# Performance work log

Measured on AMD Instinct MI355X. Metric: run time of the kernel, lower is better.

Reference implementation:

```python
import jax, jax.numpy as jnp
import numpy as np

N, E, G = 2048, 65536, 32
F_ATOM, LAT, IN, ED, NB, L = 16, 64, 128, 32, 5, 5


def setup_inputs() -> dict:
    key = jax.random.key(0)
    ks = iter(jax.random.split(key, 64))
    nxt = lambda: next(ks)
    def w(shape):
        fan_in = shape[-2] if len(shape) >= 2 else 1
        return jax.random.normal(nxt(), shape, jnp.float32) / np.sqrt(fan_in)
    inp = {}
    inp['x'] = jax.random.normal(nxt(), (N, F_ATOM), jnp.float32)
    inp['t'] = jax.random.uniform(nxt(), (G, 1), jnp.float32)
    inp['z'] = jax.random.normal(nxt(), (N, LAT), jnp.float32)
    inp['edge_index'] = jax.random.randint(nxt(), (2, E), 0, N, jnp.int32)
    inp['edge_attr'] = jax.random.normal(nxt(), (E, NB), jnp.float32)
    inp['batch'] = jnp.sort(jax.random.randint(nxt(), (N,), 0, G, jnp.int32))
    inp['batch_edge_global'] = jax.random.randint(nxt(), (E,), 0, G, jnp.int32)
    # top-level dense layers
    inp['Wt_a'] = w((1, IN)); inp['bt_a'] = jnp.zeros((IN,))
    inp['Wt_b'] = w((1, ED)); inp['bt_b'] = jnp.zeros((ED,))
    inp['W_atom'] = w((F_ATOM, IN)); inp['b_atom'] = jnp.zeros((IN,))
    inp['W_bond'] = w((NB, ED)); inp['b_bond'] = jnp.zeros((ED,))
    inp['W_lat'] = w((LAT, IN)); inp['b_lat'] = jnp.zeros((IN,))
    inp['W_at'] = w((IN, IN)); inp['b_at'] = jnp.zeros((IN,))
    inp['W_bt'] = w((ED, ED)); inp['b_bt'] = jnp.zeros((ED,))
    # TopoEdgeGNN: L layers of edge-conditioned message passing with edge update
    inp['Wmsg'] = w((L, 2 * IN + ED, IN)); inp['bmsg'] = jnp.zeros((L, IN))
    inp['Wnode'] = w((L, 2 * IN, IN)); inp['bnode'] = jnp.zeros((L, IN))
    inp['Wedge'] = w((L, 2 * IN + ED, ED)); inp['bedge'] = jnp.zeros((L, ED))
    # prediction head
    inp['Wsh'] = w((IN, IN)); inp['bsh'] = jnp.zeros((IN,))
    inp['Wbm'] = w((ED, IN)); inp['bbm'] = jnp.zeros((IN,))
    inp['Wbl'] = w((IN, NB)); inp['bbl'] = jnp.zeros((NB,))
    inp['Wal'] = w((IN, F_ATOM + LAT)); inp['bal'] = jnp.zeros((F_ATOM + LAT,))
    return inp


def reference(x, t, z, edge_index, edge_attr, batch, batch_edge_global,
              Wt_a, bt_a, Wt_b, bt_b, W_atom, b_atom, W_bond, b_bond,
              W_lat, b_lat, W_at, b_at, W_bt, b_bt,
              Wmsg, bmsg, Wnode, bnode, Wedge, bedge,
              Wsh, bsh, Wbm, bbm, Wbl, bbl, Wal, bal):
    j, i = edge_index[0], edge_index[1]
    # time embeddings, gathered to nodes / edges
    ta = t @ Wt_a + bt_a            # [G, IN]
    tb = t @ Wt_b + bt_b            # [G, ED]
    tnode = ta[batch]               # [N, IN]
    tedge = tb[batch_edge_global]   # [E, ED]
    # node features
    s = x @ W_atom + b_atom
    s = (s + tnode) @ W_at + b_at
    s = s + (z @ W_lat + b_lat)
    # edge features
    e = edge_attr @ W_bond + b_bond
    e = (e + tedge) @ W_bt + b_bt
    # TopoEdgeGNN: message passing with residual node/edge updates
    for l in range(L):
        m = jax.nn.silu(jnp.concatenate([s[i], s[j], e], -1) @ Wmsg[l] + bmsg[l])  # [E, IN]
        agg = jax.ops.segment_sum(m, i, num_segments=N)                            # [N, IN]
        s = s + jax.nn.silu(jnp.concatenate([s, agg], -1) @ Wnode[l] + bnode[l])
        e = e + jax.nn.silu(jnp.concatenate([s[i], s[j], e], -1) @ Wedge[l] + bedge[l])
    # prediction head
    s2 = jax.nn.silu(s @ Wsh + bsh)
    al = s2 @ Wal + bal
    atoms_pred, latent_pred = al[:, :F_ATOM], al[:, F_ATOM:]
    # dense edge symmetrization: scatter edges into [N, N, ED], symmetrize, gather back
    e_dense = jnp.zeros((N, N, ED), e.dtype).at[j, i].set(e)
    e_dense = 0.5 * (e_dense + e_dense.transpose(1, 0, 2))
    e_sym = e_dense[j, i]           # [E, ED]
    f = jax.nn.silu(s2[i] + s2[j] + (e_sym @ Wbm + bbm))
    bonds_pred = f @ Wbl + bbl
    return latent_pred, atoms_pred, bonds_pred
```

## Files before the change

kernel.cpp:

```cpp
#include <hip/hip_runtime.h>
#include <hip/hip_bf16.h>

#define NN 2048
#define NE 65536
#define NG 32
#define CIN 128
#define CED 32
#define CLAT 64
#define CFA 16
#define CNB 5
#define NL 5

#define OFF_AT (NN * CLAT)
#define OFF_B  (NN * CLAT + NN * CFA)

typedef __attribute__((ext_vector_type(8))) short bf16x8;
typedef __attribute__((ext_vector_type(4))) float f32x4;

__device__ __forceinline__ float silu_f(float v) { return v / (1.0f + __expf(-v)); }
__device__ __forceinline__ short f2bs(float v) {
    __hip_bfloat16 h = __float2bfloat16(v);
    return *reinterpret_cast<short*>(&h);
}
__device__ __forceinline__ float bs2f(short s) {
    return __bfloat162float(*reinterpret_cast<__hip_bfloat16*>(&s));
}
__device__ __forceinline__ unsigned pack2(float a, float b) {
    return ((unsigned)(unsigned short)f2bs(b) << 16) | (unsigned short)f2bs(a);
}
__device__ __forceinline__ unsigned addpack(unsigned ua, unsigned va) {
    float a0 = bs2f((short)(ua & 0xffff)), a1 = bs2f((short)(ua >> 16));
    float b0 = bs2f((short)(va & 0xffff)), b1 = bs2f((short)(va >> 16));
    return pack2(a0 + b0, a1 + b1);
}

struct KArgs {
    const float *x, *t, *z;
    const int *jj, *ii;
    const float *ea;
    const int *batch, *beg;
    const float *Wt_a, *bt_a, *Wt_b, *bt_b, *W_atom, *b_atom, *W_bond, *b_bond;
    const float *W_lat, *b_lat, *W_at, *b_at, *W_bt, *b_bt;
    const float *Wmsg, *bmsg, *Wnode, *bnode, *Wedge, *bedge;
    const float *Wsh, *bsh, *Wbm, *bbm, *Wbl, *bbl, *Wal, *bal;
    float *s, *e;
    float *agg;
    int *cnt, *pflag, *eflag, *rowpos, *rowstart, *invp, *i_s, *j_s;
    short *s2, *U, *V, *P, *Q;
    int *map;
    short *Wpn, *Wpsh, *Wpal, *Wpbm, *Wproj, *W3m, *We3;
    float *out;
};

__device__ __forceinline__ void phase_pack(const KArgs& a, int start, int stride)
{
    for (int idx = start; idx < 6 * 4 * 20 * 64 * 8; idx += stride) {
        int j = idx & 7, t0 = idx >> 3, lane = t0 & 63, tt = t0 >> 6;
        int kq = (lane >> 4) * 8 + j, n16 = lane & 15;
        if (idx < NL * 8 * 8 * 64 * 8) {
            int nt = tt & 7, kt = (tt >> 3) & 7, l = tt >> 6;
            a.Wpn[idx] = f2bs(a.Wnode[((size_t)l * 256 + kt * 32 + kq) * CIN + nt * 16 + n16]);
        }
        if (idx < 4 * 8 * 64 * 8) {
            int nt = tt & 7, kt = tt >> 3;
            a.Wpsh[idx] = f2bs(a.Wsh[(size_t)(kt * 32 + kq) * CIN + nt * 16 + n16]);
        }
        if (idx < 4 * 5 * 64 * 8) {
            int nt = tt % 5, kt = tt / 5;
            a.Wpal[idx] = f2bs(a.Wal[(size_t)(kt * 32 + kq) * 80 + nt * 16 + n16]);
        }
        if (idx < 8 * 64 * 8) {
            int nt = tt & 7;
            a.Wpbm[idx] = f2bs(a.Wbm[(size_t)kq * CIN + nt * 16 + n16]);
        }
        {
            int nt = tt % 20; int t2 = tt / 20; int kt = t2 & 3; int slot = t2 >> 2;
            int k = kt * 32 + kq;
            float v;
            if (nt < 16) {
                int msgl = slot % 5;
                int srcK = (nt < 8) ? k : 128 + k;
                int col = (nt & 7) * 16 + n16;
                v = a.Wmsg[((size_t)msgl * 288 + srcK) * CIN + col];
            } else {
                int edgel = (slot == 0) ? 0 : slot - 1;
                int srcK = (nt < 18) ? k : 128 + k;
                int col = (nt & 1) * 16 + n16;
                v = a.Wedge[((size_t)edgel * 288 + srcK) * CED + col];
            }
            a.Wproj[idx] = f2bs(v);
        }
        if (idx < NL * 8 * 64 * 8) {
            int nt = tt & 7, l = tt >> 3;
            a.W3m[idx] = f2bs(a.Wmsg[((size_t)l * 288 + 256 + kq) * CIN + nt * 16 + n16]);
        }
        if (idx < NL * 2 * 64 * 8) {
            int nt = tt & 1, l = tt >> 1;
            a.We3[idx] = f2bs(a.Wedge[((size_t)l * 288 + 256 + kq) * CED + nt * 16 + n16]);
        }
    }
}

__device__ __forceinline__ void phase_init_s(const KArgs& a, char* smem, int tile, int tid)
{
    float* xs  = (float*)smem;
    float* zs  = (float*)(smem + 1024);
    float* tmp = (float*)(smem + 5120);
    float* tv  = (float*)(smem + 13312);
    int nb0 = tile * 16;
    int c = tid & 127, h = tid >> 7;
    if (tid < 16 * CFA / 4) ((float4*)xs)[tid] = ((const float4*)a.x)[nb0 * (CFA / 4) + tid];
    if (tid < 16 * CLAT / 4) ((float4*)zs)[tid] = ((const float4*)a.z)[nb0 * (CLAT / 4) + tid];
    if (tid < 16) tv[tid] = a.t[a.batch[nb0 + tid]];
    __syncthreads();
    float wta = a.Wt_a[c], base0 = a.b_atom[c] + a.bt_a[c];
    float acc[8];
#pragma unroll
    for (int q = 0; q < 8; q++) acc[q] = base0 + tv[h * 8 + q] * wta;
    for (int k = 0; k < CFA; k++) {
        float w = a.W_atom[k * CIN + c];
#pragma unroll
        for (int q = 0; q < 8; q++) acc[q] += xs[(h * 8 + q) * CFA + k] * w;
    }
#pragma unroll
    for (int q = 0; q < 8; q++) tmp[(h * 8 + q) * CIN + c] = acc[q];
    __syncthreads();
    float base1 = a.b_at[c] + a.b_lat[c];
    float acc2[8];
#pragma unroll
    for (int q = 0; q < 8; q++) acc2[q] = base1;
    for (int k4 = 0; k4 < CIN / 4; k4++) {
        float w0 = a.W_at[(4 * k4 + 0) * CIN + c], w1 = a.W_at[(4 * k4 + 1) * CIN + c];
        float w2 = a.W_at[(4 * k4 + 2) * CIN + c], w3 = a.W_at[(4 * k4 + 3) * CIN + c];
#pragma unroll
        for (int q = 0; q < 8; q++) {
            float4 f = *(const float4*)&tmp[(h * 8 + q) * CIN + 4 * k4];
            acc2[q] += f.x * w0 + f.y * w1 + f.z * w2 + f.w * w3;
        }
    }
    for (int k4 = 0; k4 < CLAT / 4; k4++) {
        float w0 = a.W_lat[(4 * k4 + 0) * CIN + c], w1 = a.W_lat[(4 * k4 + 1) * CIN + c];
        float w2 = a.W_lat[(4 * k4 + 2) * CIN + c], w3 = a.W_lat[(4 * k4 + 3) * CIN + c];
#pragma unroll
        for (int q = 0; q < 8; q++) {
            float4 f = *(const float4*)&zs[(h * 8 + q) * CLAT + 4 * k4];
            acc2[q] += f.x * w0 + f.y * w1 + f.z * w2 + f.w * w3;
        }
    }
#pragma unroll
    for (int q = 0; q < 8; q++) {
        int nd = nb0 + h * 8 + q;
        a.s[(size_t)nd * CIN + c] = acc2[q];
    }
}

__device__ __forceinline__ void phase_init_e(const KArgs& a, char* smem, int tb, int tid)
{
    float* eas   = (float*)smem;
    float* tv    = (float*)(smem + 1280);
    int*   sp    = (int*)(smem + 1536);
    float* tmp   = (float*)(smem + 1792);
    float* wbt   = (float*)(smem + 10240);
    float* wbond = (float*)(smem + 14336);
    float* cb    = (float*)(smem + 14976);
    float* wtb   = (float*)(smem + 15104);
    float* bbt2  = (float*)(smem + 15232);
    int k0 = tb * 64;
    for (int idx = tid; idx < 320; idx += 256) eas[idx] = a.ea[(size_t)k0 * 5 + idx];
    if (tid < 64) { tv[tid] = a.t[a.beg[k0 + tid]]; sp[tid] = a.invp[k0 + tid]; }
    for (int idx = tid; idx < 1024; idx += 256) wbt[idx] = a.W_bt[idx];
    if (tid < 160) wbond[tid] = a.W_bond[tid];
    if (tid < 32) { cb[tid] = a.b_bond[tid] + a.bt_b[tid]; wtb[tid] = a.Wt_b[tid]; bbt2[tid] = a.b_bt[tid]; }
    __syncthreads();
    int ch = tid & 31, eg = tid >> 5;
#pragma unroll
    for (int q = 0; q < 8; q++) {
        int le = eg * 8 + q;
        float acc = cb[ch] + tv[le] * wtb[ch];
#pragma unroll
        for (int bb = 0; bb < CNB; bb++) acc += eas[le * 5 + bb] * wbond[bb * 32 + ch];
        tmp[le * 33 + ch] = acc;
    }
    __syncthreads();
#pragma unroll
    for (int q = 0; q < 8; q++) {
        int le = eg * 8 + q;
        float acc2 = bbt2[ch];
        for (int d = 0; d < 32; d++) acc2 += tmp[le * 33 + d] * wbt[d * 32 + ch];
        size_t ix = (size_t)sp[le] * CED + ch;
        a.e[ix] = acc2;
        if (ch == 0) {
            int k = k0 + le;
            atomicMax(&a.map[(size_t)a.jj[k] * NN + a.ii[k]], k);
        }
    }
}

__device__ __forceinline__ void phase_node2(
    const KArgs& a, char* smem, int tile, int tid, bool DO_NODE, bool DO_POST,
    bool LOAD_S, bool STORE_S,
    const short* Wpn_l, const float* bnode_l, const short* Wproj_slot, float (*s_reg)[4],
    const int* eflag, int gen)
{
    short* feat  = (short*)smem;
    short* feat2 = (short*)(smem + 8448);
    int nb0 = tile * 16;
    int lane = tid & 63, w = tid >> 6;
    int quad = lane >> 4, n16 = lane & 15;

    if (DO_NODE) {
        if (eflag) {
            if (tid == 0) {
                int r0 = a.rowstart[nb0];
                int ed = (nb0 + 16 < NN) ? a.rowstart[nb0 + 16] : NE;
                if (ed > r0) {
                    int t1 = (ed - 1) >> 6;
                    for (int t = r0 >> 6; t <= t1; t++)
                        while (__hip_atomic_load(&eflag[t], __ATOMIC_RELAXED, __HIP_MEMORY_SCOPE_AGENT) < gen)
                            __builtin_amdgcn_s_sleep(2);
                }
            }
            __syncthreads();
            __threadfence();
        }
#pragma unroll
        for (int n2 = 0; n2 < 2; n2++) {
            int col = (w * 2 + n2) * 16 + n16;
#pragma unroll
            for (int r = 0; r < 4; r++) {
                int row = quad * 4 + r;
                if (LOAD_S) s_reg[n2][r] = a.s[(size_t)(nb0 + row) * CIN + col];
                feat[row * 264 + col] = f2bs(s_reg[n2][r]);
            }
        }
#pragma unroll
        for (int k2 = 0; k2 < 2; k2++) {
            int idx = tid + k2 * 256;
            int kl = idx >> 5, c = idx & 31;
            size_t base = (size_t)(nb0 + kl) * 128 + c;
            float4 p0 = ((const float4*)a.agg)[base];
            float4 p1 = ((const float4*)a.agg)[base + 32];
            float4 p2 = ((const float4*)a.agg)[base + 64];
            float4 p3 = ((const float4*)a.agg)[base + 96];
            float4 v; v.x = p0.x + p1.x + p2.x + p3.x; v.y = p0.y + p1.y + p2.y + p3.y;
            v.z = p0.z + p1.z + p2.z + p3.z; v.w = p0.w + p1.w + p2.w + p3.w;
            uint2 p; p.x = pack2(v.x, v.y); p.y = pack2(v.z, v.w);
            *(uint2*)&feat[kl * 264 + 128 + 4 * c] = p;
        }
        __syncthreads();
        f32x4 acc[2];
        acc[0] = (f32x4){0.f, 0.f, 0.f, 0.f};
        acc[1] = (f32x4){0.f, 0.f, 0.f, 0.f};
        const short* fbase = feat + n16 * 264 + quad * 8;
#pragma unroll
        for (int kt = 0; kt < 8; kt++) {
            bf16x8 av = *(const bf16x8*)(fbase + kt * 32);
#pragma unroll
            for (int n2 = 0; n2 < 2; n2++) {
                int nt = w * 2 + n2;
                bf16x8 b = *(const bf16x8*)(Wpn_l + ((size_t)(kt * 8 + nt) * 64 + lane) * 8);
                acc[n2] = __builtin_amdgcn_mfma_f32_16x16x32_bf16(av, b, acc[n2], 0, 0, 0);
            }
        }
#pragma unroll
        for (int n2 = 0; n2 < 2; n2++) {
            int col = (w * 2 + n2) * 16 + n16;
            float bb = bnode_l[col];
#pragma unroll
            for (int r = 0; r < 4; r++) {
                int row = quad * 4 + r;
                float v = s_reg[n2][r] + silu_f(acc[n2][r] + bb);
                s_reg[n2][r] = v;
                if (STORE_S) a.s[(size_t)(nb0 + row) * CIN + col] = v;
                feat2[row * 136 + col] = f2bs(v);
            }
        }
        __syncthreads();
    } else {
        int kl = tid >> 4, c = tid & 15;
        const float4* sp4 = (const float4*)&a.s[(size_t)(nb0 + kl) * CIN + c * 8];
        float4 v0 = sp4[0], v1 = sp4[1];
        uint4 p; p.x = pack2(v0.x, v0.y); p.y = pack2(v0.z, v0.w);
        p.z = pack2(v1.x, v1.y); p.w = pack2(v1.z, v1.w);
        *(uint4*)&feat2[kl * 136 + c * 8] = p;
        __syncthreads();
    }

    {
        f32x4 accp[5];
#pragma unroll
        for (int t2 = 0; t2 < 5; t2++) accp[t2] = (f32x4){0.f, 0.f, 0.f, 0.f};
        const short* abase = feat2 + n16 * 136 + quad * 8;
#pragma unroll
        for (int kt = 0; kt < 4; kt++) {
            bf16x8 av = *(const bf16x8*)(abase + kt * 32);
#pragma unroll
            for (int n5 = 0; n5 < 5; n5++) {
                int nt = w * 5 + n5;
                bf16x8 b = *(const bf16x8*)(Wproj_slot + ((size_t)(kt * 20 + nt) * 64 + lane) * 8);
                accp[n5] = __builtin_amdgcn_mfma_f32_16x16x32_bf16(av, b, accp[n5], 0, 0, 0);
            }
        }
#pragma unroll
        for (int n5 = 0; n5 < 5; n5++) {
            int nt = w * 5 + n5;
#pragma unroll
            for (int r = 0; r < 4; r++) {
                int node = tile * 16 + quad * 4 + r;
                short bv = f2bs(accp[n5][r]);
                if (nt < 8)       a.U[(size_t)node * CIN + nt * 16 + n16] = bv;
                else if (nt < 16) a.V[(size_t)node * CIN + (nt - 8) * 16 + n16] = bv;
                else if (nt < 18) a.P[(size_t)node * CED + (nt - 16) * 16 + n16] = bv;
                else              a.Q[(size_t)node * CED + (nt - 18) * 16 + n16] = bv;
            }
        }
    }

    if (DO_POST) {
        short* feat_s2 = feat;
        const short* fbase = feat2 + n16 * 136 + quad * 8;
        f32x4 acc[2];
        acc[0] = (f32x4){0.f, 0.f, 0.f, 0.f};
        acc[1] = (f32x4){0.f, 0.f, 0.f, 0.f};
#pragma unroll
        for (int kt = 0; kt < 4; kt++) {
            bf16x8 av = *(const bf16x8*)(fbase + kt * 32);
#pragma unroll
            for (int n2 = 0; n2 < 2; n2++) {
                int nt = w * 2 + n2;
                bf16x8 b = *(const bf16x8*)(a.Wpsh + ((size_t)(kt * 8 + nt) * 64 + lane) * 8);
                acc[n2] = __builtin_amdgcn_mfma_f32_16x16x32_bf16(av, b, acc[n2], 0, 0, 0);
            }
        }
#pragma unroll
        for (int n2 = 0; n2 < 2; n2++) {
            int col = (w * 2 + n2) * 16 + n16;
            float bb = a.bsh[col];
#pragma unroll
            for (int r = 0; r < 4; r++) {
                int row = quad * 4 + r;
                float v = silu_f(acc[n2][r] + bb);
                short bv = f2bs(v);
                a.s2[(size_t)(nb0 + row) * CIN + col] = bv;
                feat_s2[row * 136 + col] = bv;
            }
        }
        __syncthreads();
        const short* abase2 = feat_s2 + n16 * 136 + quad * 8;
        f32x4 acca[2];
        acca[0] = (f32x4){0.f, 0.f, 0.f, 0.f};
        acca[1] = (f32x4){0.f, 0.f, 0.f, 0.f};
        int nAl = (w == 0) ? 2 : 1;
        int ntl[2] = {w, 4};
#pragma unroll
        for (int kt = 0; kt < 4; kt++) {
            bf16x8 av = *(const bf16x8*)(abase2 + kt * 32);
#pragma unroll
            for (int q = 0; q < 2; q++) {
                if (q < nAl) {
                    bf16x8 b = *(const bf16x8*)(a.Wpal + ((size_t)(kt * 5 + ntl[q]) * 64 + lane) * 8);
                    acca[q] = __builtin_amdgcn_mfma_f32_16x16x32_bf16(av, b, acca[q], 0, 0, 0);
                }
            }
        }
#pragma unroll
        for (int q = 0; q < 2; q++) {
            if (q < nAl) {
                int col = ntl[q] * 16 + n16;
                float bb = a.bal[col];
#pragma unroll
                for (int r = 0; r < 4; r++) {
                    int node = nb0 + quad * 4 + r;
                    float v = acca[q][r] + bb;
                    if (col < CFA) a.out[OFF_AT + node * CFA + col] = v;
                    else           a.out[(size_t)node * CLAT + (col - CFA)] = v;
                }
            }
        }
    }
}

__device__ __forceinline__ void phase_em2(
    const KArgs& a, char* smem, int tb, int tid, bool DO_EDGE, bool DO_MSG, bool LOAD_E, bool WRITE_E,
    const short* We3p, const float* bedge_l, const short* W3mp, const float* bmsg_l,
    float (*e_reg)[4], int* eflag, int gen)
{
    short* feat_e = (short*)smem;
    short* uv_bf  = (short*)(smem + 5120);
    short* pq_bf  = (short*)(smem + 22528);
    int*   sii    = (int*)(smem + 27648);
    int*   sjj    = (int*)(smem + 27904);
    int e0 = tb * 64;
    int lane = tid & 63, w = tid >> 6;
    int quad = lane >> 4, n16 = lane & 15;
    if (tid < 64) sii[tid] = a.i_s[e0 + tid];
    else if (tid < 128) sjj[tid - 64] = a.j_s[e0 + tid - 64];
    __syncthreads();
#pragma unroll
    for (int nt = 0; nt < 2; nt++) {
        int ch = nt * 16 + n16;
#pragma unroll
        for (int r = 0; r < 4; r++) {
            int el = w * 16 + quad * 4 + r;
            if (LOAD_E) e_reg[nt][r] = a.e[(size_t)(e0 + el) * CED + ch];
            feat_e[el * 40 + ch] = f2bs(e_reg[nt][r]);
        }
    }
    if (DO_EDGE) {
        uint2 pa[2], qb[2];
#pragma unroll
        for (int k2 = 0; k2 < 2; k2++) {
            int idx = tid + k2 * 256;
            int kl = idx >> 3, c = idx & 7;
            pa[k2] = ((const uint2*)a.P)[(size_t)sii[kl] * 8 + c];
            qb[k2] = ((const uint2*)a.Q)[(size_t)sjj[kl] * 8 + c];
        }
#pragma unroll
        for (int k2 = 0; k2 < 2; k2++) {
            int idx = tid + k2 * 256;
            int kl = idx >> 3, c = idx & 7;
            uint2 o; o.x = addpack(pa[k2].x, qb[k2].x); o.y = addpack(pa[k2].y, qb[k2].y);
            *(uint2*)&pq_bf[kl * 40 + 4 * c] = o;
        }
    }
    if (DO_MSG) {
        uint4 ua[4], va[4];
#pragma unroll
        for (int k2 = 0; k2 < 4; k2++) {
            int idx = tid + k2 * 256;
            int kl = idx >> 4, c = idx & 15;
            ua[k2] = ((const uint4*)a.U)[(size_t)sii[kl] * 16 + c];
            va[k2] = ((const uint4*)a.V)[(size_t)sjj[kl] * 16 + c];
        }
#pragma unroll
        for (int k2 = 0; k2 < 4; k2++) {
            int idx = tid + k2 * 256;
            int kl = idx >> 4, c = idx & 15;
            uint4 o; o.x = addpack(ua[k2].x, va[k2].x); o.y = addpack(ua[k2].y, va[k2].y);
            o.z = addpack(ua[k2].z, va[k2].z); o.w = addpack(ua[k2].w, va[k2].w);
            *(uint4*)&uv_bf[kl * 136 + c * 8] = o;
        }
    }
    __syncthreads();
    const short* abase = feat_e + (w * 16 + n16) * 40 + quad * 8;
    bf16x8 av = *(const bf16x8*)abase;

    if (DO_EDGE) {
        f32x4 acc_e[2];
        acc_e[0] = (f32x4){0.f, 0.f, 0.f, 0.f};
        acc_e[1] = (f32x4){0.f, 0.f, 0.f, 0.f};
#pragma unroll
        for (int nt = 0; nt < 2; nt++) {
            bf16x8 b = *(const bf16x8*)(We3p + ((size_t)(nt * 64 + lane)) * 8);
            acc_e[nt] = __builtin_amdgcn_mfma_f32_16x16x32_bf16(av, b, acc_e[nt], 0, 0, 0);
        }
#pragma unroll
        for (int nt = 0; nt < 2; nt++) {
            int ch = nt * 16 + n16;
            float bb = bedge_l[ch];
#pragma unroll
            for (int r = 0; r < 4; r++) {
                int el = w * 16 + quad * 4 + r;
                float v = e_reg[nt][r] + silu_f(acc_e[nt][r] + bb + bs2f(pq_bf[el * 40 + ch]));
                e_reg[nt][r] = v;
                feat_e[el * 40 + ch] = f2bs(v);
                if (WRITE_E) a.e[(size_t)(e0 + el) * CED + ch] = v;
            }
        }
        av = *(const bf16x8*)abase;
    }

    if (DO_MSG) {
        f32x4 acc_m[8];
#pragma unroll
        for (int t2 = 0; t2 < 8; t2++) acc_m[t2] = (f32x4){0.f, 0.f, 0.f, 0.f};
#pragma unroll
        for (int nt = 0; nt < 8; nt++) {
            bf16x8 b = *(const bf16x8*)(W3mp + ((size_t)(nt * 64 + lane)) * 8);
            acc_m[nt] = __builtin_amdgcn_mfma_f32_16x16x32_bf16(av, b, acc_m[nt], 0, 0, 0);
        }
#pragma unroll
        for (int nt = 0; nt < 8; nt++) {
            int ch = nt * 16 + n16;
            float bb = bmsg_l[ch];
#pragma unroll
            for (int r = 0; r < 4; r++) {
                int el = w * 16 + quad * 4 + r;
                int lix = el * 136 + ch;
                float m = silu_f(acc_m[nt][r] + bb + bs2f(uv_bf[lix]));
                uv_bf[lix] = f2bs(m);
            }
        }
        __syncthreads();
        if (tid < 128) {
            int c = tid;
            float run = 0.f;
            int cur = sii[0];
            for (int r = 0; r < 64; r++) {
                int tg = sii[r];
                if (tg != cur) {
                    int slot = tb - (a.rowstart[cur] >> 6); slot = (slot > 3) ? 3 : slot;
                    a.agg[((size_t)cur * 4 + slot) * CIN + c] = run;
                    run = 0.f; cur = tg;
                }
                run += bs2f(uv_bf[r * 136 + c]);
            }
            int slot = tb - (a.rowstart[cur] >> 6); slot = (slot > 3) ? 3 : slot;
            a.agg[((size_t)cur * 4 + slot) * CIN + c] = run;
        }
        if (eflag) {
            __syncthreads();
            if (tid == 0) {
                __threadfence();
                __hip_atomic_store(&eflag[tb], gen, __ATOMIC_RELAXED, __HIP_MEMORY_SCOPE_AGENT);
            }
        }
    }
}

__device__ __forceinline__ void phase_post_edge(const KArgs& a, char* smem, int tb, int tid)
{
    short* esym  = (short*)smem;
    short* sbias = (short*)(smem + 5120);
    int* sii = (int*)(smem + 22016);
    int* sjj = (int*)(smem + 22272);
    int* skf = (int*)(smem + 22528);
    int* skb = (int*)(smem + 22784);
    int e0 = tb * 64;
    if (tid < 64) sii[tid] = a.ii[e0 + tid];
    else if (tid < 128) sjj[tid - 64] = a.jj[e0 + tid - 64];
    __syncthreads();
    if (tid < 64) skf[tid] = a.invp[a.map[(size_t)sjj[tid] * NN + sii[tid]]];
    else if (tid < 128) {
        int m = a.map[(size_t)sii[tid - 64] * NN + sjj[tid - 64]];
        skb[tid - 64] = (m >= 0) ? a.invp[m] : -1;
    }
    __syncthreads();
    {
        float4 av2[2], bv2[2];
#pragma unroll
        for (int k2 = 0; k2 < 2; k2++) {
            int idx = tid + k2 * 256;
            int kl = idx >> 3, c = idx & 7;
            av2[k2] = ((const float4*)a.e)[(size_t)skf[kl] * 8 + c];
            int kb = skb[kl];
            bv2[k2] = (float4){0.f, 0.f, 0.f, 0.f};
            if (kb >= 0) bv2[k2] = ((const float4*)a.e)[(size_t)kb * 8 + c];
        }
#pragma unroll
        for (int k2 = 0; k2 < 2; k2++) {
            int idx = tid + k2 * 256;
            int kl = idx >> 3, c = idx & 7;
            uint2 p; p.x = pack2(0.5f * (av2[k2].x + bv2[k2].x), 0.5f * (av2[k2].y + bv2[k2].y));
            p.y = pack2(0.5f * (av2[k2].z + bv2[k2].z), 0.5f * (av2[k2].w + bv2[k2].w));
            *(uint2*)&esym[kl * 40 + 4 * c] = p;
        }
    }
#pragma unroll
    for (int half = 0; half < 2; half++) {
        uint2 av4[4], bv4[4];
#pragma unroll
        for (int k2 = 0; k2 < 4; k2++) {
            int idx = tid + (half * 4 + k2) * 256;
            int kl = idx >> 5, c = idx & 31;
            av4[k2] = ((const uint2*)a.s2)[(size_t)sii[kl] * 32 + c];
            bv4[k2] = ((const uint2*)a.s2)[(size_t)sjj[kl] * 32 + c];
        }
#pragma unroll
        for (int k2 = 0; k2 < 4; k2++) {
            int idx = tid + (half * 4 + k2) * 256;
            int kl = idx >> 5, c = idx & 31;
            uint2 o; o.x = addpack(av4[k2].x, bv4[k2].x); o.y = addpack(av4[k2].y, bv4[k2].y);
            *(uint2*)&sbias[kl * 132 + 4 * c] = o;
        }
    }
    __syncthreads();
    int lane = tid & 63, w = tid >> 6;
    int quad = lane >> 4, n16 = lane & 15;
    bf16x8 av = *(const bf16x8*)(esym + (w * 16 + n16) * 40 + quad * 8);
    f32x4 acc[8];
#pragma unroll
    for (int nt = 0; nt < 8; nt++) {
        bf16x8 b = *(const bf16x8*)(a.Wpbm + ((size_t)nt * 64 + lane) * 8);
        f32x4 zero = {0.f, 0.f, 0.f, 0.f};
        acc[nt] = __builtin_amdgcn_mfma_f32_16x16x32_bf16(av, b, zero, 0, 0, 0);
    }
    float f[8][4];
#pragma unroll
    for (int nt = 0; nt < 8; nt++) {
        int col = nt * 16 + n16;
        float bb = a.bbm[col];
#pragma unroll
        for (int r = 0; r < 4; r++) {
            int row = w * 16 + quad * 4 + r;
            f[nt][r] = silu_f(acc[nt][r] + bb + bs2f(sbias[row * 132 + col]));
        }
    }
    __syncthreads();
    short* fshT = sbias;
#pragma unroll
    for (int nt = 0; nt < 8; nt++) {
        int col = nt * 16 + n16;
#pragma unroll
        for (int r = 0; r < 4; r++) {
            int row = w * 16 + quad * 4 + r;
            fshT[col * 66 + row] = f2bs(f[nt][r]);
        }
    }
    __syncthreads();
    for (int idx = tid; idx < 64 * CNB; idx += 256) {
        int kl = idx / CNB, b = idx - kl * CNB;
        float acc3 = a.bbl[b];
        for (int d = 0; d < CIN; d++) acc3 += bs2f(fshT[d * 66 + kl]) * a.Wbl[d * CNB + b];
        a.out[OFF_B + (size_t)(e0 + kl) * CNB + b] = acc3;
    }
}

__global__ __launch_bounds__(256) void k_prologue(KArgs a)
{
    __shared__ __align__(16) char smem[13440];
    int b = blockIdx.x, tid = threadIdx.x;
    if (b < 960) phase_pack(a, b * 256 + tid, 960 * 256);
    else if (b < 1088) phase_init_s(a, smem, b - 960, tid);
    else {
        int base = (b - 1088) * 1024;
#pragma unroll
        for (int q = 0; q < 4; q++) atomicAdd(&a.cnt[a.ii[base + q * 256 + tid]], 1);
    }
}
__global__ __launch_bounds__(256) void k_prefix(KArgs a)
{
    __shared__ int part[256];
    int tid = threadIdx.x;
    int loc[8], sum = 0;
#pragma unroll
    for (int q = 0; q < 8; q++) { loc[q] = a.cnt[tid * 8 + q]; sum += loc[q]; }
    part[tid] = sum;
    __syncthreads();
    if (tid == 0) { int r = 0; for (int i = 0; i < 256; i++) { int v = part[i]; part[i] = r; r += v; } }
    __syncthreads();
    int r = part[tid];
#pragma unroll
    for (int q = 0; q < 8; q++) { a.rowpos[tid * 8 + q] = r; a.rowstart[tid * 8 + q] = r; r += loc[q]; }
}
__global__ void k_perm(KArgs a)
{
    int k = blockIdx.x * 256 + threadIdx.x;
    int iv = a.ii[k];
    int p = atomicAdd(&a.rowpos[iv], 1);
    a.invp[k] = p;
    a.i_s[p] = iv;
    a.j_s[p] = a.jj[k];
}
__global__ __launch_bounds__(256) void k_initE(KArgs a)
{
    __shared__ __align__(16) char smem[15360];
    int bid = blockIdx.x, tid = threadIdx.x;
    if (bid < 1024) {
        phase_init_e(a, smem, bid, tid);
    } else {
        float s_reg[2][4];
        phase_node2(a, smem, bid - 1024, tid, false, false, false, false,
                    nullptr, nullptr, a.Wproj, s_reg, nullptr, 0);
    }
}

__global__ __launch_bounds__(256, 5) void k_layer(KArgs a, int gen, int de, int dm,
        const short* We3p, const float* bedge_l, const short* W3mp, const float* bmsg_l,
        const short* Wpn_l, const float* bnode_l, const short* Wproj_slot, int dopost)
{
    __shared__ __align__(16) char smem[28160];
    int bid = blockIdx.x, tid = threadIdx.x;
    if (bid < 1024) {
        float e_reg[2][4];
        phase_em2(a, smem, bid, tid, de != 0, dm != 0, true, de != 0,
                  We3p, bedge_l, W3mp, bmsg_l, e_reg, a.eflag, gen);
    } else {
        float s_reg[2][4];
        phase_node2(a, smem, bid - 1024, tid, true, dopost != 0, true, true,
                    Wpn_l, bnode_l, Wproj_slot, s_reg, a.eflag, gen);
    }
}

__global__ __launch_bounds__(256) void k_init_e(KArgs a)
{
    __shared__ __align__(16) char smem[15360];
    phase_init_e(a, smem, blockIdx.x, threadIdx.x);
}
__global__ __launch_bounds__(256) void k_node_proj(KArgs a, int donode, int dopost,
                                                   const short* Wpn_l, const float* bnode_l,
                                                   const short* Wproj_slot)
{
    __shared__ __align__(16) char smem[12800];
    float s_reg[2][4];
    phase_node2(a, smem, blockIdx.x, threadIdx.x, donode != 0, dopost != 0,
                donode != 0, donode != 0, Wpn_l, bnode_l, Wproj_slot, s_reg, nullptr, 0);
}
__global__ __launch_bounds__(256) void k_em(KArgs a, int de, int dm, const short* We3p,
                                            const float* bedge_l, const short* W3mp, const float* bmsg_l)
{
    __shared__ __align__(16) char smem[28160];
    float e_reg[2][4];
    phase_em2(a, smem, blockIdx.x, threadIdx.x, de != 0, dm != 0, true, de != 0,
              We3p, bedge_l, W3mp, bmsg_l, e_reg, nullptr, 0);
}
__global__ __launch_bounds__(256) void k_post_edge(KArgs a)
{
    __shared__ __align__(16) char smem[23040];
    phase_post_edge(a, smem, blockIdx.x, threadIdx.x);
}

extern "C" void kernel_launch(void* const* d_in, const int* in_sizes, int n_in,
                              void* d_out, int out_size, void* d_ws, size_t ws_size,
                              hipStream_t stream) {
    KArgs a;
    a.x      = (const float*)d_in[0];
    a.t      = (const float*)d_in[1];
    a.z      = (const float*)d_in[2];
    const int* eidx = (const int*)d_in[3];
    a.jj     = eidx;
    a.ii     = eidx + NE;
    a.ea     = (const float*)d_in[4];
    a.batch  = (const int*)d_in[5];
    a.beg    = (const int*)d_in[6];
    a.Wt_a   = (const float*)d_in[7];
    a.bt_a   = (const float*)d_in[8];
    a.Wt_b   = (const float*)d_in[9];
    a.bt_b   = (const float*)d_in[10];
    a.W_atom = (const float*)d_in[11];
    a.b_atom = (const float*)d_in[12];
    a.W_bond = (const float*)d_in[13];
    a.b_bond = (const float*)d_in[14];
    a.W_lat  = (const float*)d_in[15];
    a.b_lat  = (const float*)d_in[16];
    a.W_at   = (const float*)d_in[17];
    a.b_at   = (const float*)d_in[18];
    a.W_bt   = (const float*)d_in[19];
    a.b_bt   = (const float*)d_in[20];
    a.Wmsg   = (const float*)d_in[21];
    a.bmsg   = (const float*)d_in[22];
    a.Wnode  = (const float*)d_in[23];
    a.bnode  = (const float*)d_in[24];
    a.Wedge  = (const float*)d_in[25];
    a.bedge  = (const float*)d_in[26];
    a.Wsh    = (const float*)d_in[27];
    a.bsh    = (const float*)d_in[28];
    a.Wbm    = (const float*)d_in[29];
    a.bbm    = (const float*)d_in[30];
    a.Wbl    = (const float*)d_in[31];
    a.bbl    = (const float*)d_in[32];
    a.Wal    = (const float*)d_in[33];
    a.bal    = (const float*)d_in[34];

    a.s        = (float*)d_ws;
    a.e        = a.s + (size_t)NN * CIN;
    a.agg      = a.e + (size_t)NE * CED;
    a.cnt      = (int*)(a.agg + (size_t)NN * 4 * CIN);
    a.pflag    = a.cnt + NN;
    a.eflag    = a.pflag + 256;
    a.rowpos   = a.eflag + 1024;
    a.rowstart = a.rowpos + NN;
    a.invp     = a.rowstart + NN;
    a.i_s      = a.invp + NE;
    a.j_s      = a.i_s + NE;
    a.s2       = (short*)(a.j_s + NE);
    a.U        = a.s2 + (size_t)NN * CIN;
    a.V        = a.U + (size_t)NN * CIN;
    a.P        = a.V + (size_t)NN * CIN;
    a.Q        = a.P + (size_t)NN * CED;
    a.map      = (int*)(a.Q + (size_t)NN * CED);
    a.Wpn      = (short*)(a.map + (size_t)NN * NN);
    a.Wpsh     = a.Wpn + (size_t)NL * 8 * 8 * 64 * 8;
    a.Wpal     = a.Wpsh + (size_t)4 * 8 * 64 * 8;
    a.Wpbm     = a.Wpal + (size_t)4 * 5 * 64 * 8;
    a.Wproj    = a.Wpbm + (size_t)8 * 64 * 8;
    a.W3m      = a.Wproj + (size_t)6 * 4 * 20 * 64 * 8;
    a.We3      = a.W3m + (size_t)NL * 8 * 64 * 8;
    a.out      = (float*)d_out;

    static int mode = -1;
    if (mode < 0) {
        int dev = 0;
        (void)hipGetDevice(&dev);
        hipDeviceProp_t props;
        int ncu = 0;
        if (hipGetDeviceProperties(&props, dev) == hipSuccess) ncu = props.multiProcessorCount;
        int m1 = 0;
        if (hipOccupancyMaxActiveBlocksPerMultiprocessor(&m1, k_layer, 256, 0) != hipSuccess) m1 = 0;
        mode = ((long)m1 * ncu >= 1152) ? 1 : 0;
    }

    hipMemsetAsync(a.map, 0xFF, (size_t)NN * NN * sizeof(int), stream);
    hipMemsetAsync(a.agg, 0,
                   (size_t)NN * 4 * CIN * sizeof(float) + (NN + 256 + 1024) * sizeof(int),
                   stream);

    k_prologue<<<1152, 256, 0, stream>>>(a);
    k_prefix<<<1, 256, 0, stream>>>(a);
    k_perm<<<NE / 256, 256, 0, stream>>>(a);
    k_initE<<<1152, 256, 0, stream>>>(a);

    if (mode) {
        for (int k = 0; k < NL; k++) {
            int de = (k > 0) ? 1 : 0;
            k_layer<<<1152, 256, 0, stream>>>(a, k + 1, de, 1,
                de ? a.We3 + (size_t)(k - 1) * 2 * 64 * 8 : a.We3,
                de ? a.bedge + (k - 1) * CED : a.bedge,
                a.W3m + (size_t)k * 8 * 64 * 8, a.bmsg + k * CIN,
                a.Wpn + (size_t)k * 8 * 8 * 64 * 8, a.bnode + k * CIN,
                a.Wproj + (size_t)(k + 1) * 4 * 20 * 64 * 8, (k == NL - 1) ? 1 : 0);
        }
        k_layer<<<1024, 256, 0, stream>>>(a, NL + 1, 1, 0,
            a.We3 + (size_t)(NL - 1) * 2 * 64 * 8, a.bedge + (NL - 1) * CED,
            a.W3m, a.bmsg, a.Wpn, a.bnode, a.Wproj, 0);
    } else {
        k_em<<<NE / 64, 256, 0, stream>>>(a, 0, 1, nullptr, nullptr, a.W3m, a.bmsg);
        for (int l = 0; l < NL; l++) {
            int dopost = (l == NL - 1) ? 1 : 0;
            k_node_proj<<<NN / 16, 256, 0, stream>>>(a, 1, dopost,
                a.Wpn + (size_t)l * 8 * 8 * 64 * 8, a.bnode + l * CIN,
                a.Wproj + (size_t)(l + 1) * 4 * 20 * 64 * 8);
            int dm = (l < NL - 1) ? 1 : 0;
            k_em<<<NE / 64, 256, 0, stream>>>(a, 1, dm,
                a.We3 + (size_t)l * 2 * 64 * 8, a.bedge + l * CED,
                dm ? a.W3m + (size_t)(l + 1) * 8 * 64 * 8 : a.W3m,
                dm ? a.bmsg + (l + 1) * CIN : a.bmsg);
        }
    }
    k_post_edge<<<NE / 64, 256, 0, stream>>>(a);
}
```

Before: 339.0 us.

## Pre-scatter V/Q rows into edge-sorted order via j-sorted producer blocks

Adds a scatter phase that reads node projections V and Q grouped by source node j and writes them into per-edge contiguous buffers in the i-sorted edge order. The edge/message phase can then read those rows sequentially instead of doing random gathers by j. Node tiles publish per-tile flags so scatter blocks can start while other nodes are still updating, and double buffers keep layers apart. This adds large extra workspace traffic (an NE×CIN bf16 write plus read per layer), more blocks per fused layer launch, and a stricter occupancy threshold for choosing the fused mode.

```diff
diff --git a/kernel.cpp b/kernel.cpp
--- a/kernel.cpp
+++ b/kernel.cpp
@@ -32,6 +32,9 @@
     float a0 = bs2f((short)(ua & 0xffff)), a1 = bs2f((short)(ua >> 16));
     float b0 = bs2f((short)(va & 0xffff)), b1 = bs2f((short)(va >> 16));
     return pack2(a0 + b0, a1 + b1);
+}
+__device__ __forceinline__ unsigned long long ld_sc64(const unsigned long long* p) {
+    return __hip_atomic_load(p, __ATOMIC_RELAXED, __HIP_MEMORY_SCOPE_AGENT);
 }
 
 struct KArgs {
@@ -45,10 +48,12 @@
     const float *Wsh, *bsh, *Wbm, *bbm, *Wbl, *bbl, *Wal, *bal;
     float *s, *e;
     float *agg;
-    int *cnt, *pflag, *eflag, *rowpos, *rowstart, *invp, *i_s, *j_s;
+    int *cnt, *pflag, *eflag, *cnt2, *nflag, *rowpos, *rowpos2, *rowstart, *invp, *i_s, *j_s;
+    int *j_s2, *tgt2;
     short *s2, *U, *V, *P, *Q;
     int *map;
     short *Wpn, *Wpsh, *Wpal, *Wpbm, *Wproj, *W3m, *We3;
+    short *uvt0, *pqt0;
     float *out;
 };
 
@@ -196,11 +201,58 @@
     }
 }
 
+__device__ __forceinline__ void phase_vscatter(const KArgs& a, char* smem, int tb, int tid,
+                                               short* uvt, short* pqt, const int* nflag, int gen)
+{
+    int* js = (int*)smem;
+    int* tg = (int*)(smem + 256);
+    int e0 = tb * 64;
+    if (tid < 64) js[tid] = a.j_s2[e0 + tid];
+    else if (tid < 128) tg[tid - 64] = a.tgt2[e0 + tid - 64];
+    __syncthreads();
+    if (nflag) {
+        if (tid == 0) {
+            int t0 = js[0] >> 4, t1 = js[63] >> 4;
+            for (int t = t0; t <= t1; t++)
+                while (__hip_atomic_load(&nflag[t * 16], __ATOMIC_RELAXED, __HIP_MEMORY_SCOPE_AGENT) < gen)
+                    __builtin_amdgcn_s_sleep(2);
+        }
+        __syncthreads();
+        asm volatile("" ::: "memory");
+    }
+    unsigned long long vv[8];
+#pragma unroll
+    for (int k2 = 0; k2 < 8; k2++) {
+        int idx = tid + k2 * 256;
+        int kl = idx >> 5, c = idx & 31;
+        vv[k2] = ld_sc64((const unsigned long long*)a.V + (size_t)js[kl] * 32 + c);
+    }
+    unsigned long long qq[2];
+#pragma unroll
+    for (int k2 = 0; k2 < 2; k2++) {
+        int idx = tid + k2 * 256;
+        int kl = idx >> 3, c = idx & 7;
+        qq[k2] = ld_sc64((const unsigned long long*)a.Q + (size_t)js[kl] * 8 + c);
+    }
+#pragma unroll
+    for (int k2 = 0; k2 < 8; k2++) {
+        int idx = tid + k2 * 256;
+        int kl = idx >> 5, c = idx & 31;
+        ((unsigned long long*)uvt)[(size_t)tg[kl] * 32 + c] = vv[k2];
+    }
+#pragma unroll
+    for (int k2 = 0; k2 < 2; k2++) {
+        int idx = tid + k2 * 256;
+        int kl = idx >> 3, c = idx & 7;
+        ((unsigned long long*)pqt)[(size_t)tg[kl] * 8 + c] = qq[k2];
+    }
+}
+
 __device__ __forceinline__ void phase_node2(
     const KArgs& a, char* smem, int tile, int tid, bool DO_NODE, bool DO_POST,
     bool LOAD_S, bool STORE_S,
     const short* Wpn_l, const float* bnode_l, const short* Wproj_slot, float (*s_reg)[4],
-    const int* eflag, int gen)
+    const int* eflag, int gen, int* nflag, int ngen)
 {
     short* feat  = (short*)smem;
     short* feat2 = (short*)(smem + 8448);
@@ -316,6 +368,14 @@
         }
     }
 
+    if (nflag) {
+        __syncthreads();
+        if (tid == 0) {
+            __threadfence();
+            __hip_atomic_store(&nflag[tile * 16], ngen, __ATOMIC_RELAXED, __HIP_MEMORY_SCOPE_AGENT);
+        }
+    }
+
     if (DO_POST) {
         short* feat_s2 = feat;
         const short* fbase = feat2 + n16 * 136 + quad * 8;
@@ -383,7 +443,7 @@
 __device__ __forceinline__ void phase_em2(
     const KArgs& a, char* smem, int tb, int tid, bool DO_EDGE, bool DO_MSG, bool LOAD_E, bool WRITE_E,
     const short* We3p, const float* bedge_l, const short* W3mp, const float* bmsg_l,
-    float (*e_reg)[4], int* eflag, int gen)
+    float (*e_reg)[4], int* eflag, int gen, const short* uvt, const short* pqt)
 {
     short* feat_e = (short*)smem;
     short* uv_bf  = (short*)(smem + 5120);
@@ -413,7 +473,8 @@
             int idx = tid + k2 * 256;
             int kl = idx >> 3, c = idx & 7;
             pa[k2] = ((const uint2*)a.P)[(size_t)sii[kl] * 8 + c];
-            qb[k2] = ((const uint2*)a.Q)[(size_t)sjj[kl] * 8 + c];
+            qb[k2] = pqt ? ((const uint2*)pqt)[(size_t)(e0 + kl) * 8 + c]
+                         : ((const uint2*)a.Q)[(size_t)sjj[kl] * 8 + c];
         }
 #pragma unroll
         for (int k2 = 0; k2 < 2; k2++) {
@@ -430,7 +491,8 @@
             int idx = tid + k2 * 256;
             int kl = idx >> 4, c = idx & 15;
             ua[k2] = ((const uint4*)a.U)[(size_t)sii[kl] * 16 + c];
-            va[k2] = ((const uint4*)a.V)[(size_t)sjj[kl] * 16 + c];
+            va[k2] = uvt ? ((const uint4*)uvt)[(size_t)(e0 + kl) * 16 + c]
+                         : ((const uint4*)a.V)[(size_t)sjj[kl] * 16 + c];
         }
 #pragma unroll
         for (int k2 = 0; k2 < 4; k2++) {
@@ -622,28 +684,39 @@
     int b = blockIdx.x, tid = threadIdx.x;
     if (b < 960) phase_pack(a, b * 256 + tid, 960 * 256);
     else if (b < 1088) phase_init_s(a, smem, b - 960, tid);
-    else {
+    else if (b < 1152) {
         int base = (b - 1088) * 1024;
 #pragma unroll
         for (int q = 0; q < 4; q++) atomicAdd(&a.cnt[a.ii[base + q * 256 + tid]], 1);
-    }
-}
-__global__ __launch_bounds__(256) void k_prefix(KArgs a)
+    } else {
+        int base = (b - 1152) * 1024;
+#pragma unroll
+        for (int q = 0; q < 4; q++) atomicAdd(&a.cnt2[a.jj[base + q * 256 + tid]], 1);
+    }
+}
+__global__ __launch_bounds__(256) void k_prefix(KArgs a, int vs)
 {
     __shared__ int part[256];
-    int tid = threadIdx.x;
+    int b = blockIdx.x, tid = threadIdx.x;
+    if (b == 1 && !vs) return;
+    const int* src = b ? a.cnt2 : a.cnt;
+    int* dst = b ? a.rowpos2 : a.rowpos;
     int loc[8], sum = 0;
 #pragma unroll
-    for (int q = 0; q < 8; q++) { loc[q] = a.cnt[tid * 8 + q]; sum += loc[q]; }
+    for (int q = 0; q < 8; q++) { loc[q] = src[tid * 8 + q]; sum += loc[q]; }
     part[tid] = sum;
     __syncthreads();
     if (tid == 0) { int r = 0; for (int i = 0; i < 256; i++) { int v = part[i]; part[i] = r; r += v; } }
     __syncthreads();
     int r = part[tid];
 #pragma unroll
-    for (int q = 0; q < 8; q++) { a.rowpos[tid * 8 + q] = r; a.rowstart[tid * 8 + q] = r; r += loc[q]; }
-}
-__global__ void k_perm(KArgs a)
+    for (int q = 0; q < 8; q++) {
+        dst[tid * 8 + q] = r;
+        if (!b) a.rowstart[tid * 8 + q] = r;
+        r += loc[q];
+    }
+}
+__global__ void k_perm(KArgs a, int vs)
 {
     int k = blockIdx.x * 256 + threadIdx.x;
     int iv = a.ii[k];
@@ -651,34 +724,44 @@
     a.invp[k] = p;
     a.i_s[p] = iv;
     a.j_s[p] = a.jj[k];
-}
-__global__ __launch_bounds__(256) void k_initE(KArgs a)
+    if (vs) {
+        int jv = a.jj[k];
+        int p2 = atomicAdd(&a.rowpos2[jv], 1);
+        a.j_s2[p2] = jv;
+        a.tgt2[p2] = p;
+    }
+}
+__global__ __launch_bounds__(256) void k_initE(KArgs a, int vs)
 {
     __shared__ __align__(16) char smem[15360];
     int bid = blockIdx.x, tid = threadIdx.x;
-    if (bid < 1024) {
-        phase_init_e(a, smem, bid, tid);
-    } else {
+    if (bid < 1024) phase_init_e(a, smem, bid, tid);
+    else if (bid < 1152) {
         float s_reg[2][4];
         phase_node2(a, smem, bid - 1024, tid, false, false, false, false,
-                    nullptr, nullptr, a.Wproj, s_reg, nullptr, 0);
-    }
-}
-
-__global__ __launch_bounds__(256, 5) void k_layer(KArgs a, int gen, int de, int dm,
+                    nullptr, nullptr, a.Wproj, s_reg, nullptr, 0, vs ? a.nflag : nullptr, 1);
+    } else {
+        phase_vscatter(a, smem, bid - 1152, tid, a.uvt0, a.pqt0, a.nflag, 1);
+    }
+}
+__global__ __launch_bounds__(256, 5) void k_layer(KArgs a, int gen, int ngen, int de, int dm,
         const short* We3p, const float* bedge_l, const short* W3mp, const float* bmsg_l,
-        const short* Wpn_l, const float* bnode_l, const short* Wproj_slot, int dopost)
+        const short* Wpn_l, const float* bnode_l, const short* Wproj_slot, int dopost,
+        const short* uvt_r, const short* pqt_r, short* uvt_w, short* pqt_w)
 {
     __shared__ __align__(16) char smem[28160];
     int bid = blockIdx.x, tid = threadIdx.x;
     if (bid < 1024) {
         float e_reg[2][4];
         phase_em2(a, smem, bid, tid, de != 0, dm != 0, true, de != 0,
-                  We3p, bedge_l, W3mp, bmsg_l, e_reg, a.eflag, gen);
-    } else {
+                  We3p, bedge_l, W3mp, bmsg_l, e_reg, a.eflag, gen, uvt_r, pqt_r);
+    } else if (bid < 1152) {
         float s_reg[2][4];
         phase_node2(a, smem, bid - 1024, tid, true, dopost != 0, true, true,
-                    Wpn_l, bnode_l, Wproj_slot, s_reg, a.eflag, gen);
+                    Wpn_l, bnode_l, Wproj_slot, s_reg, a.eflag, gen,
+                    ngen ? a.nflag : nullptr, ngen);
+    } else {
+        phase_vscatter(a, smem, bid - 1152, tid, uvt_w, pqt_w, a.nflag, ngen);
     }
 }
 
@@ -686,6 +769,11 @@
 {
     __shared__ __align__(16) char smem[15360];
     phase_init_e(a, smem, blockIdx.x, threadIdx.x);
+}
+__global__ __launch_bounds__(256) void k_vscat(KArgs a, short* uvt, short* pqt)
+{
+    __shared__ __align__(16) char smem[512];
+    phase_vscatter(a, smem, blockIdx.x, threadIdx.x, uvt, pqt, nullptr, 0);
 }
 __global__ __launch_bounds__(256) void k_node_proj(KArgs a, int donode, int dopost,
                                                    const short* Wpn_l, const float* bnode_l,
@@ -694,15 +782,18 @@
     __shared__ __align__(16) char smem[12800];
     float s_reg[2][4];
     phase_node2(a, smem, blockIdx.x, threadIdx.x, donode != 0, dopost != 0,
-                donode != 0, donode != 0, Wpn_l, bnode_l, Wproj_slot, s_reg, nullptr, 0);
+                donode != 0, donode != 0, Wpn_l, bnode_l, Wproj_slot, s_reg, nullptr, 0,
+                nullptr, 0);
 }
 __global__ __launch_bounds__(256) void k_em(KArgs a, int de, int dm, const short* We3p,
-                                            const float* bedge_l, const short* W3mp, const float* bmsg_l)
+                                            const float* bedge_l, const short* W3mp,
+                                            const float* bmsg_l,
+                                            const short* uvt_r, const short* pqt_r)
 {
     __shared__ __align__(16) char smem[28160];
     float e_reg[2][4];
     phase_em2(a, smem, blockIdx.x, threadIdx.x, de != 0, dm != 0, true, de != 0,
-              We3p, bedge_l, W3mp, bmsg_l, e_reg, nullptr, 0);
+              We3p, bedge_l, W3mp, bmsg_l, e_reg, nullptr, 0, uvt_r, pqt_r);
 }
 __global__ __launch_bounds__(256) void k_post_edge(KArgs a)
 {
@@ -758,12 +849,17 @@
     a.cnt      = (int*)(a.agg + (size_t)NN * 4 * CIN);
     a.pflag    = a.cnt + NN;
     a.eflag    = a.pflag + 256;
-    a.rowpos   = a.eflag + 1024;
-    a.rowstart = a.rowpos + NN;
+    a.cnt2     = a.eflag + 1024;
+    a.nflag    = a.cnt2 + NN;
+    a.rowpos   = a.nflag + 2048;
+    a.rowpos2  = a.rowpos + NN;
+    a.rowstart = a.rowpos2 + NN;
     a.invp     = a.rowstart + NN;
     a.i_s      = a.invp + NE;
     a.j_s      = a.i_s + NE;
-    a.s2       = (short*)(a.j_s + NE);
+    a.j_s2     = a.j_s + NE;
+    a.tgt2     = a.j_s2 + NE;
+    a.s2       = (short*)(a.tgt2 + NE);
     a.U        = a.s2 + (size_t)NN * CIN;
     a.V        = a.U + (size_t)NN * CIN;
     a.P        = a.V + (size_t)NN * CIN;
@@ -776,7 +872,14 @@
     a.Wproj    = a.Wpbm + (size_t)8 * 64 * 8;
     a.W3m      = a.Wproj + (size_t)6 * 4 * 20 * 64 * 8;
     a.We3      = a.W3m + (size_t)NL * 8 * 64 * 8;
+    a.uvt0     = a.We3 + (size_t)NL * 2 * 64 * 8;
+    a.pqt0     = a.uvt0 + (size_t)2 * NE * CIN;
     a.out      = (float*)d_out;
+
+    const size_t UVS = (size_t)NE * CIN;
+    const size_t PQS = (size_t)NE * CED;
+    size_t need = (size_t)((char*)(a.pqt0 + 2 * PQS) - (char*)d_ws);
+    int use_vs = (ws_size >= need) ? 1 : 0;
 
     static int mode = -1;
     if (mode < 0) {
@@ -787,45 +890,61 @@
         if (hipGetDeviceProperties(&props, dev) == hipSuccess) ncu = props.multiProcessorCount;
         int m1 = 0;
         if (hipOccupancyMaxActiveBlocksPerMultiprocessor(&m1, k_layer, 256, 0) != hipSuccess) m1 = 0;
-        mode = ((long)m1 * ncu >= 1152) ? 1 : 0;
-    }
+        mode = ((long)m1 * ncu >= 1280) ? 1 : 0;
+    }
+
+    short* uvb[2] = { a.uvt0, a.uvt0 + UVS };
+    short* pqb[2] = { a.pqt0, a.pqt0 + PQS };
 
     hipMemsetAsync(a.map, 0xFF, (size_t)NN * NN * sizeof(int), stream);
     hipMemsetAsync(a.agg, 0,
-                   (size_t)NN * 4 * CIN * sizeof(float) + (NN + 256 + 1024) * sizeof(int),
+                   (size_t)NN * 4 * CIN * sizeof(float) +
+                   (NN + 256 + 1024 + NN + 2048) * sizeof(int),
                    stream);
 
-    k_prologue<<<1152, 256, 0, stream>>>(a);
-    k_prefix<<<1, 256, 0, stream>>>(a);
-    k_perm<<<NE / 256, 256, 0, stream>>>(a);
-    k_initE<<<1152, 256, 0, stream>>>(a);
+    k_prologue<<<use_vs ? 1216 : 1152, 256, 0, stream>>>(a);
+    k_prefix<<<2, 256, 0, stream>>>(a, use_vs);
+    k_perm<<<NE / 256, 256, 0, stream>>>(a, use_vs);
 
     if (mode) {
+        k_initE<<<use_vs ? 2176 : 1152, 256, 0, stream>>>(a, use_vs);
         for (int k = 0; k < NL; k++) {
             int de = (k > 0) ? 1 : 0;
-            k_layer<<<1152, 256, 0, stream>>>(a, k + 1, de, 1,
+            const short* ur = use_vs ? uvb[k & 1] : nullptr;
+            const short* pr = use_vs ? pqb[k & 1] : nullptr;
+            k_layer<<<use_vs ? 2176 : 1152, 256, 0, stream>>>(a, k + 1, use_vs ? (k + 2) : 0,
+                de, 1,
                 de ? a.We3 + (size_t)(k - 1) * 2 * 64 * 8 : a.We3,
                 de ? a.bedge + (k - 1) * CED : a.bedge,
                 a.W3m + (size_t)k * 8 * 64 * 8, a.bmsg + k * CIN,
                 a.Wpn + (size_t)k * 8 * 8 * 64 * 8, a.bnode + k * CIN,
-                a.Wproj + (size_t)(k + 1) * 4 * 20 * 64 * 8, (k == NL - 1) ? 1 : 0);
-        }
-        k_layer<<<1024, 256, 0, stream>>>(a, NL + 1, 1, 0,
+                a.Wproj + (size_t)(k + 1) * 4 * 20 * 64 * 8, (k == NL - 1) ? 1 : 0,
+                ur, pr, uvb[(k + 1) & 1], pqb[(k + 1) & 1]);
+        }
+        k_layer<<<1024, 256, 0, stream>>>(a, NL + 1, 0, 1, 0,
             a.We3 + (size_t)(NL - 1) * 2 * 64 * 8, a.bedge + (NL - 1) * CED,
-            a.W3m, a.bmsg, a.Wpn, a.bnode, a.Wproj, 0);
+            a.W3m, a.bmsg, a.Wpn, a.bnode, a.Wproj, 0,
+            use_vs ? uvb[1] : nullptr, use_vs ? pqb[1] : nullptr, nullptr, nullptr);
     } else {
-        k_em<<<NE / 64, 256, 0, stream>>>(a, 0, 1, nullptr, nullptr, a.W3m, a.bmsg);
-        for (int l = 0; l < NL; l++) {
-            int dopost = (l == NL - 1) ? 1 : 0;
-            k_node_proj<<<NN / 16, 256, 0, stream>>>(a, 1, dopost,
-                a.Wpn + (size_t)l * 8 * 8 * 64 * 8, a.bnode + l * CIN,
-                a.Wproj + (size_t)(l + 1) * 4 * 20 * 64 * 8);
-            int dm = (l < NL - 1) ? 1 : 0;
-            k_em<<<NE / 64, 256, 0, stream>>>(a, 1, dm,
-                a.We3 + (size_t)l * 2 * 64 * 8, a.bedge + l * CED,
-                dm ? a.W3m + (size_t)(l + 1) * 8 * 64 * 8 : a.W3m,
-                dm ? a.bmsg + (l + 1) * CIN : a.bmsg);
-        }
+        k_init_e<<<1024, 256, 0, stream>>>(a);
+        k_node_proj<<<NN / 16, 256, 0, stream>>>(a, 0, 0, nullptr, nullptr, a.Wproj);
+        if (use_vs) k_vscat<<<1024, 256, 0, stream>>>(a, uvb[0], pqb[0]);
+        for (int k = 0; k < NL; k++) {
+            int de = (k > 0) ? 1 : 0;
+            k_em<<<1024, 256, 0, stream>>>(a, de, 1,
+                de ? a.We3 + (size_t)(k - 1) * 2 * 64 * 8 : a.We3,
+                de ? a.bedge + (k - 1) * CED : a.bedge,
+                a.W3m + (size_t)k * 8 * 64 * 8, a.bmsg + k * CIN,
+                use_vs ? uvb[k & 1] : nullptr, use_vs ? pqb[k & 1] : nullptr);
+            k_node_proj<<<NN / 16, 256, 0, stream>>>(a, 1, (k == NL - 1) ? 1 : 0,
+                a.Wpn + (size_t)k * 8 * 8 * 64 * 8, a.bnode + k * CIN,
+                a.Wproj + (size_t)(k + 1) * 4 * 20 * 64 * 8);
+            if (use_vs) k_vscat<<<1024, 256, 0, stream>>>(a, uvb[(k + 1) & 1], pqb[(k + 1) & 1]);
+        }
+        k_em<<<1024, 256, 0, stream>>>(a, 1, 0,
+            a.We3 + (size_t)(NL - 1) * 2 * 64 * 8, a.bedge + (NL - 1) * CED,
+            a.W3m, a.bmsg,
+            use_vs ? uvb[1] : nullptr, use_vs ? pqb[1] : nullptr);
     }
     k_post_edge<<<NE / 64, 256, 0, stream>>>(a);
 }
```

Measured after the change: 395.1 us. 16.6% more time.
